# Kernel tuning notes

Measured on AMD Instinct MI355X. Metric: run time of the kernel, lower is better.

Reference implementation:

```python
import jax, jax.numpy as jnp
import numpy as np

NUM_SAMPLES = 1024


def _cdist(a, b):
    # a, b: (n, 3) -> (n, n) pairwise euclidean distances (torch.cdist p=2)
    d2 = jnp.sum((a[:, None, :] - b[None, :, :]) ** 2, axis=-1)
    return jnp.sqrt(jnp.maximum(d2, 0.0))


def _greedy_match_cost(cost):
    # Greedy sequential matching: repeatedly take the global argmin over
    # still-unmatched rows/cols, accumulate its cost, eliminate row+col.
    n = cost.shape[0]

    def step(carry, _):
        row_mask, col_mask, loss = carry
        valid = row_mask[:, None] & col_mask[None, :]
        masked = jnp.where(valid, cost, jnp.inf)
        idx = jnp.argmin(masked)  # row-major first-min == torch's min(dim=1)+argmin tiebreak
        r = idx // n
        c = idx % n
        loss = loss + cost[r, c]
        return (row_mask.at[r].set(False), col_mask.at[c].set(False), loss), None

    init = (jnp.ones((n,), dtype=bool), jnp.ones((n,), dtype=bool), jnp.float32(0.0))
    (_, _, loss), _ = jax.lax.scan(step, init, None, length=n)
    return loss / n


def setup_inputs() -> dict:
    key = jax.random.key(0)
    k1, k2, k3 = jax.random.split(key, 3)
    B, N, n = 8, 4096, NUM_SAMPLES
    S1 = jax.random.normal(k1, (B, N, 3), dtype=jnp.float32)
    S2 = jax.random.normal(k2, (B, N, 3), dtype=jnp.float32)
    # torch.randperm(N)[:n] per batch element: without-replacement sampling
    perm_keys = jax.random.split(k3, B)
    indices = jax.vmap(lambda k: jax.random.permutation(k, N)[:n])(perm_keys).astype(jnp.int32)
    return {"S1": S1, "S2": S2, "indices": indices}


def reference(S1, S2, indices):
    # sample the same indices from both sets, per batch (matches original loop)
    s1 = jnp.take_along_axis(S1, indices[:, :, None], axis=1)  # (B, n, 3)
    s2 = jnp.take_along_axis(S2, indices[:, :, None], axis=1)  # (B, n, 3)
    cost = jax.vmap(_cdist)(s1, s2)  # (B, n, n)
    losses = jax.vmap(_greedy_match_cost)(cost)  # (B,)
    return jnp.mean(losses)
```

## Files before the change

kernel.cpp:

```cpp
#include <hip/hip_runtime.h>
#include <stdint.h>

#define BATCH 8
#define NPTS 4096
#define NS 1024
#define KD 6

typedef unsigned long long u64;
typedef unsigned int u32;
typedef unsigned short u16;
typedef unsigned char u8;

#define DEADV (~0ull)
#define QNANB 0x7FC00000u

__device__ __forceinline__ float pdist3(float ax, float ay, float az,
                                        float bx, float by, float bz) {
    float dx = ax - bx, dy = ay - by, dz = az - bz;
    float d2 = __fmaf_rn(dz, dz, __fmaf_rn(dy, dy, dx * dx));
    return __fsqrt_rn(d2);
}

__device__ __forceinline__ u64 packv(float d, u32 row, u32 col) {
    return ((u64)__float_as_uint(d) << 20) | ((u64)row << 10) | (u64)col;
}

__device__ __forceinline__ u64 u64min2(u64 a, u64 b) { return a < b ? a : b; }
__device__ __forceinline__ u64 u64max2(u64 a, u64 b) { return a > b ? a : b; }

__device__ __forceinline__ u64 tree16(const u64* p) {
    u64 a0 = u64min2(p[0], p[1]),   a1 = u64min2(p[2], p[3]);
    u64 a2 = u64min2(p[4], p[5]),   a3 = u64min2(p[6], p[7]);
    u64 a4 = u64min2(p[8], p[9]),   a5 = u64min2(p[10], p[11]);
    u64 a6 = u64min2(p[12], p[13]), a7 = u64min2(p[14], p[15]);
    u64 b0 = u64min2(a0, a1), b1 = u64min2(a2, a3);
    u64 b2 = u64min2(a4, a5), b3 = u64min2(a6, a7);
    return u64min2(u64min2(b0, b1), u64min2(b2, b3));
}

template<int CTRL>
__device__ __forceinline__ u64 dpp_min_step(u64 m) {
    u32 lo = (u32)m, hi = (u32)(m >> 32);
    u32 olo = (u32)__builtin_amdgcn_update_dpp(-1, (int)lo, CTRL, 0xF, 0xF, false);
    u32 ohi = (u32)__builtin_amdgcn_update_dpp(-1, (int)hi, CTRL, 0xF, 0xF, false);
    u64 o = ((u64)ohi << 32) | olo;
    return o < m ? o : m;
}

__device__ __forceinline__ u64 wave_min_u64(u64 m) {
    m = dpp_min_step<0x111>(m);
    m = dpp_min_step<0x112>(m);
    m = dpp_min_step<0x114>(m);
    m = dpp_min_step<0x118>(m);
    m = dpp_min_step<0x142>(m);
    m = dpp_min_step<0x143>(m);
    u32 lo = (u32)__builtin_amdgcn_readlane((int)(u32)m, 63);
    u32 hi = (u32)__builtin_amdgcn_readlane((int)(u32)(m >> 32), 63);
    return ((u64)hi << 32) | lo;
}

__global__ void gather_k(const float* __restrict__ S1, const float* __restrict__ S2,
                         const int* __restrict__ idx,
                         float4* __restrict__ s1g, float4* __restrict__ s2g,
                         int* __restrict__ cnt) {
    int t = blockIdx.x * blockDim.x + threadIdx.x;
    if (t == 0) *cnt = 0;
    if (t >= BATCH * NS) return;
    int b = t >> 10;
    int j = idx[t];
    const float* p1 = S1 + ((size_t)b * NPTS + j) * 3;
    const float* p2 = S2 + ((size_t)b * NPTS + j) * 3;
    s1g[t] = make_float4(p1[0], p1[1], p1[2], 0.f);
    s2g[t] = make_float4(p2[0], p2[1], p2[2], 0.f);
}

__global__ void lists_k(const float4* __restrict__ s1g, const float4* __restrict__ s2g,
                        u64* __restrict__ rlist_g, u64* __restrict__ clist_g) {
    __shared__ float4 pts[NS];
    int gg = blockIdx.x * 4 + (threadIdx.x >> 6);
    int lane = threadIdx.x & 63;
    int side = (gg >= BATCH * NS) ? 1 : 0;
    int g = gg - side * (BATCH * NS);
    int b = g >> 10;
    u32 rc = (u32)(g & 1023);
    const float4* other = (side ? s1g : s2g) + (size_t)b * NS;
    for (int i = threadIdx.x; i < NS; i += 256) pts[i] = other[i];
    float4 a = side ? s2g[g] : s1g[g];
    __syncthreads();
    u64 cand[16];
    #pragma unroll
    for (int k = 0; k < 16; ++k) {
        int o = lane + (k << 6);
        float4 q = pts[o];
        float d = pdist3(a.x, a.y, a.z, q.x, q.y, q.z);
        cand[k] = side ? packv(d, (u32)o, rc) : packv(d, rc, (u32)o);
    }
    u64* out = (side ? clist_g : rlist_g) + (size_t)b * NS * KD + rc;
    for (int i = 0; i < KD; ++i) {
        u64 m1 = wave_min_u64(tree16(cand));
        if (lane == 0) out[(size_t)i * NS] = m1;
        #pragma unroll
        for (int k = 0; k < 16; ++k) cand[k] = (cand[k] == m1) ? DEADV : cand[k];
    }
}

__global__ void __launch_bounds__(1024, 1)
resolve_k(const float4* __restrict__ s1g, const float4* __restrict__ s2g,
          const u64* __restrict__ rlist_gl, const u64* __restrict__ clist_gl,
          float* __restrict__ loss_ws, int* __restrict__ cnt,
          float* __restrict__ out, u64* __restrict__ instr) {
    __shared__ u64 rlist[KD * NS];
    __shared__ u64 clist[KD * NS];
    __shared__ u64 rmin[NS];
    __shared__ u64 cmin[NS];
    __shared__ float4 s1p[NS];
    __shared__ float4 s2p[NS];
    __shared__ u8 rptrs[NS], cptrs[NS];
    __shared__ u16 qrow[NS], qcol[NS];
    __shared__ u16 lrows[NS], lcols[NS];
    __shared__ float lred[1024];
    __shared__ int qrn, qcn, matched, nlr, nlc, stale_n;
    int b = blockIdx.x;
    int tid = threadIdx.x;
    int lane = tid & 63, wv = tid >> 6;

    {
        const float4* rs = (const float4*)(rlist_gl + (size_t)b * NS * KD);
        const float4* cs = (const float4*)(clist_gl + (size_t)b * NS * KD);
        float4* rd = (float4*)rlist;
        float4* cd = (float4*)clist;
        for (int i = tid; i < NS * KD / 2; i += 1024) { rd[i] = rs[i]; cd[i] = cs[i]; }
    }
    s1p[tid] = s1g[(size_t)b * NS + tid];
    s2p[tid] = s2g[(size_t)b * NS + tid];
    rptrs[tid] = 1; cptrs[tid] = 1;
    lrows[tid] = (u16)tid; lcols[tid] = (u16)tid;
    if (tid == 0) { matched = 0; stale_n = NS; }
    __syncthreads();
    rmin[tid] = rlist[tid];
    cmin[tid] = clist[tid];
    float loss = 0.f;
    __syncthreads();

    long long tmark = 0;
    u64 sA = 0, sB = 0;
    if (tid == 0) tmark = clock64();

    for (int round = 0; round < NS; ++round) {
        u64 myk = rmin[tid];
        u32 c = (u32)myk & 1023u;
        bool mut = (myk != DEADV) && (cmin[c] == myk);
        if (mut) {
            loss += __uint_as_float((u32)(myk >> 20));
            rmin[tid] = DEADV;
            cmin[c] = DEADV;
            s1p[tid].x = __uint_as_float(QNANB);
            s2p[c].x   = __uint_as_float(QNANB);
        }
        u64 bal = __ballot((int)mut);
        if (lane == 0 && bal) atomicAdd(&matched, (int)__popcll(bal));
        if (tid == 0) { qrn = 0; qcn = 0; nlr = 0; nlc = 0; }
        __syncthreads();
        if (tid == 0) { long long t = clock64(); sA += (u64)(t - tmark); tmark = t; }
        int m = matched;
        if (m >= NS) break;
        int live = NS - m;
        int stale = stale_n;
        bool rebuild = (stale * 4 > live * 5 + 64);
        bool needR = false, needC = false;
        u64 rk = rmin[tid];
        if (rk != DEADV) {
            float pr = s2p[(u32)rk & 1023u].x;
            if (pr != pr) {
                u32 p = rptrs[tid];
                bool found = false;
                while (p < KD) {
                    u64 e = rlist[p * NS + tid];
                    ++p;
                    if (e != DEADV) {
                        float q = s2p[(u32)e & 1023u].x;
                        if (q == q) { rmin[tid] = e; found = true; break; }
                    }
                }
                rptrs[tid] = (u8)p;
                needR = !found;
            }
        }
        u64 ck = cmin[tid];
        if (ck != DEADV) {
            float pr = s1p[((u32)ck >> 10) & 1023u].x;
            if (pr != pr) {
                u32 p = cptrs[tid];
                bool found = false;
                while (p < KD) {
                    u64 e = clist[p * NS + tid];
                    ++p;
                    if (e != DEADV) {
                        float q = s1p[((u32)e >> 10) & 1023u].x;
                        if (q == q) { cmin[tid] = e; found = true; break; }
                    }
                }
                cptrs[tid] = (u8)p;
                needC = !found;
            }
        }
        {
            u64 rb2 = __ballot((int)needR);
            if (rb2) {
                int rrank = (int)__popcll(rb2 & ((1ull << lane) - 1ull));
                int rbase = 0;
                if (lane == 0) rbase = atomicAdd(&qrn, (int)__popcll(rb2));
                rbase = __shfl(rbase, 0, 64);
                if (needR) qrow[rbase + rrank] = (u16)tid;
            }
            u64 cb2 = __ballot((int)needC);
            if (cb2) {
                int crank = (int)__popcll(cb2 & ((1ull << lane) - 1ull));
                int cbase = 0;
                if (lane == 0) cbase = atomicAdd(&qcn, (int)__popcll(cb2));
                cbase = __shfl(cbase, 0, 64);
                if (needC) qcol[cbase + crank] = (u16)tid;
            }
        }
        if (rebuild) {
            float cx = s2p[tid].x;
            bool calive = (cx == cx);
            u64 cb = __ballot((int)calive);
            int crank = (int)__popcll(cb & ((1ull << lane) - 1ull));
            int cbase = 0;
            if (lane == 0) cbase = atomicAdd(&nlc, (int)__popcll(cb));
            cbase = __shfl(cbase, 0, 64);
            if (calive) lcols[cbase + crank] = (u16)tid;

            float rx = s1p[tid].x;
            bool ralive = (rx == rx);
            u64 rb = __ballot((int)ralive);
            int rrank = (int)__popcll(rb & ((1ull << lane) - 1ull));
            int rbase = 0;
            if (lane == 0) rbase = atomicAdd(&nlr, (int)__popcll(rb));
            rbase = __shfl(rbase, 0, 64);
            if (ralive) lrows[rbase + rrank] = (u16)tid;
        }
        __syncthreads();
        if (tid == 0) { long long t = clock64(); sB += (u64)(t - tmark); tmark = t; }
        int nr = qrn, nc = qcn;
        int scan_n = rebuild ? live : stale;
        if (rebuild && tid == 0) stale_n = live;
        int tot = nr + nc;
        for (int qi = wv; qi < tot; qi += 16) {
            if (qi < nr) {
                u32 r = qrow[qi];
                float4 a = s1p[r];
                u64 m1 = DEADV, m2 = DEADV;
                for (int i = lane; i < scan_n; i += 64) {
                    int cc = lcols[i];
                    float4 q = s2p[cc];
                    float d = pdist3(a.x, a.y, a.z, q.x, q.y, q.z);
                    u64 p = packv(d, r, (u32)cc);
                    u64 mx = u64max2(p, m1);
                    m1 = u64min2(m1, p);
                    m2 = u64min2(m2, mx);
                }
                u64 M1 = wave_min_u64(m1);
                u64 c2 = (m1 == M1) ? m2 : m1;
                u64 M2 = wave_min_u64(c2);
                if (lane == 0) {
                    rmin[r] = M1;
                    rlist[(KD - 1) * NS + r] = M2;
                    rptrs[r] = KD - 1;
                }
            } else {
                u32 cc = qcol[qi - nr];
                float4 a = s2p[cc];
                u64 m1 = DEADV, m2 = DEADV;
                for (int i = lane; i < scan_n; i += 64) {
                    int r = lrows[i];
                    float4 q = s1p[r];
                    float d = pdist3(q.x, q.y, q.z, a.x, a.y, a.z);
                    u64 p = packv(d, (u32)r, cc);
                    u64 mx = u64max2(p, m1);
                    m1 = u64min2(m1, p);
                    m2 = u64min2(m2, mx);
                }
                u64 M1 = wave_min_u64(m1);
                u64 c2 = (m1 == M1) ? m2 : m1;
                u64 M2 = wave_min_u64(c2);
                if (lane == 0) {
                    cmin[cc] = M1;
                    clist[(KD - 1) * NS + cc] = M2;
                    cptrs[cc] = KD - 1;
                }
            }
        }
        __syncthreads();
        if (tid == 0) tmark = clock64();
    }

    if (instr && b == 0 && tid == 0) {
        u64 n1 = sA >> 13; if (n1 > 63) n1 = 63;
        u64 n2 = sB >> 13; if (n2 > 63) n2 = 63;
        int n = (int)(n1 * 64 + n2);
        for (int k = 0; k < n; ++k)
            __builtin_nontemporal_store(0ull, instr + (size_t)k * 8);
    }

    lred[tid] = loss;
    __syncthreads();
    #pragma unroll
    for (int s = 512; s > 0; s >>= 1) {
        if (tid < s) lred[tid] += lred[tid + s];
        __syncthreads();
    }
    if (tid == 0) {
        atomicExch(&loss_ws[b], lred[0] * (1.0f / NS));
        __threadfence();
        int old = atomicAdd(cnt, 1);
        if (old == BATCH - 1) {
            __threadfence();
            float s = 0.f;
            for (int i = 0; i < BATCH; ++i) s += atomicAdd(&loss_ws[i], 0.0f);
            out[0] = s * (1.0f / BATCH);
        }
    }
}

extern "C" void kernel_launch(void* const* d_in, const int* in_sizes, int n_in,
                              void* d_out, int out_size, void* d_ws, size_t ws_size,
                              hipStream_t stream) {
    const float* S1 = (const float*)d_in[0];
    const float* S2 = (const float*)d_in[1];
    const int* idx  = (const int*)d_in[2];
    char* ws = (char*)d_ws;
    size_t o = 0;
    float4* s1g    = (float4*)(ws + o); o += (size_t)BATCH * NS * 16;
    float4* s2g    = (float4*)(ws + o); o += (size_t)BATCH * NS * 16;
    u64* rlist_g   = (u64*)(ws + o);    o += (size_t)BATCH * NS * KD * 8;
    u64* clist_g   = (u64*)(ws + o);    o += (size_t)BATCH * NS * KD * 8;
    float* loss_ws = (float*)(ws + o);  o += (size_t)BATCH * 4;
    int* cnt       = (int*)(ws + o);    o += 64;
    o = (o + 4095) & ~(size_t)4095;
    u64* instr     = (u64*)(ws + o);
    o += (size_t)4096 * 64;
    u64* instr_p = (ws_size >= o) ? instr : (u64*)0;

    gather_k<<<(BATCH * NS + 255) / 256, 256, 0, stream>>>(S1, S2, idx, s1g, s2g, cnt);
    lists_k<<<2 * BATCH * NS / 4, 256, 0, stream>>>(s1g, s2g, rlist_g, clist_g);
    resolve_k<<<BATCH, 1024, 0, stream>>>(s1g, s2g, rlist_g, clist_g, loss_ws, cnt,
                                          (float*)d_out, instr_p);
}
```

Measured before the change: 198.9 us.

## Store candidate lists as 16-bit indices and deepen lists to sixteen entries

Per-row and per-column nearest-candidate lists now hold only the partner index as u16, not packed 64-bit distance keys. Distances are recomputed from the shared point coordinates when a candidate is promoted. The smaller entries let each list grow from 6 to 16 within similar shared memory, which should cut how often a full rescan is needed when a list runs out. The cost is extra distance arithmetic on promotion and more work in lists_k to extract 16 minima per point.

```diff
diff --git a/kernel.cpp b/kernel.cpp
--- a/kernel.cpp
+++ b/kernel.cpp
@@ -4,7 +4,7 @@
 #define BATCH 8
 #define NPTS 4096
 #define NS 1024
-#define KD 6
+#define KD 16
 
 typedef unsigned long long u64;
 typedef unsigned int u32;
@@ -13,6 +13,7 @@
 
 #define DEADV (~0ull)
 #define QNANB 0x7FC00000u
+#define NOIDX 0xFFFFu
 
 __device__ __forceinline__ float pdist3(float ax, float ay, float az,
                                         float bx, float by, float bz) {
@@ -75,7 +76,7 @@
 }
 
 __global__ void lists_k(const float4* __restrict__ s1g, const float4* __restrict__ s2g,
-                        u64* __restrict__ rlist_g, u64* __restrict__ clist_g) {
+                        u16* __restrict__ rlist_g, u16* __restrict__ clist_g) {
     __shared__ float4 pts[NS];
     int gg = blockIdx.x * 4 + (threadIdx.x >> 6);
     int lane = threadIdx.x & 63;
@@ -95,10 +96,11 @@
         float d = pdist3(a.x, a.y, a.z, q.x, q.y, q.z);
         cand[k] = side ? packv(d, (u32)o, rc) : packv(d, rc, (u32)o);
     }
-    u64* out = (side ? clist_g : rlist_g) + (size_t)b * NS * KD + rc;
+    u16* out = (side ? clist_g : rlist_g) + (size_t)b * NS * KD + rc;
     for (int i = 0; i < KD; ++i) {
         u64 m1 = wave_min_u64(tree16(cand));
-        if (lane == 0) out[(size_t)i * NS] = m1;
+        if (lane == 0)
+            out[(size_t)i * NS] = side ? (u16)((m1 >> 10) & 1023u) : (u16)(m1 & 1023u);
         #pragma unroll
         for (int k = 0; k < 16; ++k) cand[k] = (cand[k] == m1) ? DEADV : cand[k];
     }
@@ -106,11 +108,11 @@
 
 __global__ void __launch_bounds__(1024, 1)
 resolve_k(const float4* __restrict__ s1g, const float4* __restrict__ s2g,
-          const u64* __restrict__ rlist_gl, const u64* __restrict__ clist_gl,
+          const u16* __restrict__ rlist_gl, const u16* __restrict__ clist_gl,
           float* __restrict__ loss_ws, int* __restrict__ cnt,
           float* __restrict__ out, u64* __restrict__ instr) {
-    __shared__ u64 rlist[KD * NS];
-    __shared__ u64 clist[KD * NS];
+    __shared__ __align__(16) u16 rlist[KD * NS];
+    __shared__ __align__(16) u16 clist[KD * NS];
     __shared__ u64 rmin[NS];
     __shared__ u64 cmin[NS];
     __shared__ float4 s1p[NS];
@@ -129,7 +131,7 @@
         const float4* cs = (const float4*)(clist_gl + (size_t)b * NS * KD);
         float4* rd = (float4*)rlist;
         float4* cd = (float4*)clist;
-        for (int i = tid; i < NS * KD / 2; i += 1024) { rd[i] = rs[i]; cd[i] = cs[i]; }
+        for (int i = tid; i < NS * KD * 2 / 16; i += 1024) { rd[i] = rs[i]; cd[i] = cs[i]; }
     }
     s1p[tid] = s1g[(size_t)b * NS + tid];
     s2p[tid] = s2g[(size_t)b * NS + tid];
@@ -137,8 +139,14 @@
     lrows[tid] = (u16)tid; lcols[tid] = (u16)tid;
     if (tid == 0) { matched = 0; stale_n = NS; }
     __syncthreads();
-    rmin[tid] = rlist[tid];
-    cmin[tid] = clist[tid];
+    {
+        u16 h = rlist[tid];
+        float4 a = s1p[tid], q = s2p[h];
+        rmin[tid] = packv(pdist3(a.x, a.y, a.z, q.x, q.y, q.z), (u32)tid, (u32)h);
+        u16 hc = clist[tid];
+        float4 a2 = s2p[tid], q2 = s1p[hc];
+        cmin[tid] = packv(pdist3(q2.x, q2.y, q2.z, a2.x, a2.y, a2.z), (u32)hc, (u32)tid);
+    }
     float loss = 0.f;
     __syncthreads();
 
@@ -172,14 +180,19 @@
         if (rk != DEADV) {
             float pr = s2p[(u32)rk & 1023u].x;
             if (pr != pr) {
+                float4 a = s1p[tid];
                 u32 p = rptrs[tid];
                 bool found = false;
                 while (p < KD) {
-                    u64 e = rlist[p * NS + tid];
+                    u16 e = rlist[p * NS + tid];
                     ++p;
-                    if (e != DEADV) {
-                        float q = s2p[(u32)e & 1023u].x;
-                        if (q == q) { rmin[tid] = e; found = true; break; }
+                    if (e != NOIDX) {
+                        float4 q = s2p[e];
+                        if (q.x == q.x) {
+                            rmin[tid] = packv(pdist3(a.x, a.y, a.z, q.x, q.y, q.z),
+                                              (u32)tid, (u32)e);
+                            found = true; break;
+                        }
                     }
                 }
                 rptrs[tid] = (u8)p;
@@ -190,14 +203,19 @@
         if (ck != DEADV) {
             float pr = s1p[((u32)ck >> 10) & 1023u].x;
             if (pr != pr) {
+                float4 a = s2p[tid];
                 u32 p = cptrs[tid];
                 bool found = false;
                 while (p < KD) {
-                    u64 e = clist[p * NS + tid];
+                    u16 e = clist[p * NS + tid];
                     ++p;
-                    if (e != DEADV) {
-                        float q = s1p[((u32)e >> 10) & 1023u].x;
-                        if (q == q) { cmin[tid] = e; found = true; break; }
+                    if (e != NOIDX) {
+                        float4 q = s1p[e];
+                        if (q.x == q.x) {
+                            cmin[tid] = packv(pdist3(q.x, q.y, q.z, a.x, a.y, a.z),
+                                              (u32)e, (u32)tid);
+                            found = true; break;
+                        }
                     }
                 }
                 cptrs[tid] = (u8)p;
@@ -266,7 +284,8 @@
                 u64 M2 = wave_min_u64(c2);
                 if (lane == 0) {
                     rmin[r] = M1;
-                    rlist[(KD - 1) * NS + r] = M2;
+                    rlist[(KD - 1) * NS + r] =
+                        (M2 == DEADV) ? (u16)NOIDX : (u16)(M2 & 1023u);
                     rptrs[r] = KD - 1;
                 }
             } else {
@@ -287,7 +306,8 @@
                 u64 M2 = wave_min_u64(c2);
                 if (lane == 0) {
                     cmin[cc] = M1;
-                    clist[(KD - 1) * NS + cc] = M2;
+                    clist[(KD - 1) * NS + cc] =
+                        (M2 == DEADV) ? (u16)NOIDX : (u16)((M2 >> 10) & 1023u);
                     cptrs[cc] = KD - 1;
                 }
             }
@@ -334,8 +354,8 @@
     size_t o = 0;
     float4* s1g    = (float4*)(ws + o); o += (size_t)BATCH * NS * 16;
     float4* s2g    = (float4*)(ws + o); o += (size_t)BATCH * NS * 16;
-    u64* rlist_g   = (u64*)(ws + o);    o += (size_t)BATCH * NS * KD * 8;
-    u64* clist_g   = (u64*)(ws + o);    o += (size_t)BATCH * NS * KD * 8;
+    u16* rlist_g   = (u16*)(ws + o);    o += (size_t)BATCH * NS * KD * 2;
+    u16* clist_g   = (u16*)(ws + o);    o += (size_t)BATCH * NS * KD * 2;
     float* loss_ws = (float*)(ws + o);  o += (size_t)BATCH * 4;
     int* cnt       = (int*)(ws + o);    o += 64;
     o = (o + 4095) & ~(size_t)4095;
```

Result: slower. 231.6 us (+16.4%).
